# Performance work log

Hardware: AMD Instinct MI355X
Metric: run time of the kernel (lower is better)

Reference implementation:

```python
import jax, jax.numpy as jnp
import numpy as np
from jax import lax

B_SZ, N_CH, N_T = 512, 129, 250
D_MODEL = 128
D_INNER = 256            # expand * d_model
D_STATE = 16
D_CONV = 4
HEADDIM = 64             # mamba_ssm default
NHEADS = D_INNER // HEADDIM  # 4
CONV_DIM = D_INNER + 2 * D_STATE        # 288 (ngroups=1)
D_IN_PROJ = 2 * D_INNER + 2 * D_STATE + NHEADS  # 548
EPS = 1e-5


def setup_inputs() -> dict:
    key = jax.random.key(0)
    ks = jax.random.split(key, 12)
    g = lambda k, shp, s: jax.random.normal(k, shp, jnp.float32) * s
    dt0 = jax.random.uniform(ks[4], (NHEADS,), minval=0.001, maxval=0.1)
    return {
        "x": jax.random.normal(ks[0], (B_SZ, N_CH, N_T), jnp.float32),
        "mixer_w": g(ks[1], (D_MODEL, N_CH), 0.05),
        "mixer_b": jnp.zeros((D_MODEL,), jnp.float32),
        "in_proj_w": g(ks[2], (D_IN_PROJ, D_MODEL), 0.05),
        "conv_w": g(ks[3], (CONV_DIM, D_CONV), 0.2),
        "conv_b": jnp.zeros((CONV_DIM,), jnp.float32),
        "dt_bias": jnp.log(jnp.expm1(dt0)),               # inverse-softplus init
        "A_log": jnp.log(jax.random.uniform(ks[5], (NHEADS,), minval=1.0, maxval=16.0)),
        "D": jnp.ones((NHEADS,), jnp.float32),
        "norm_w": jnp.ones((D_INNER,), jnp.float32),
        "out_proj_w": g(ks[6], (D_MODEL, D_INNER), 0.05),
        "head_w": g(ks[7], (1, D_MODEL), 0.05),
        "head_b": jnp.zeros((1,), jnp.float32),
    }


def reference(x, mixer_w, mixer_b, in_proj_w, conv_w, conv_b, dt_bias,
              A_log, D, norm_w, out_proj_w, head_w, head_b):
    bsz, _, T = x.shape
    # channel mixer: (B, C, T) -> (B, T, d_model)
    u = jnp.einsum('bct,dc->btd', x, mixer_w) + mixer_b
    # Mamba2 in_proj (no bias)
    zxbcdt = u @ in_proj_w.T                        # (B, T, 548)
    z = zxbcdt[..., :D_INNER]                       # gate
    xBC = zxbcdt[..., D_INNER:D_INNER + CONV_DIM]   # (B, T, 288)
    dt = jax.nn.softplus(zxbcdt[..., -NHEADS:] + dt_bias)  # (B, T, H)
    # causal depthwise conv1d (kernel 4) + SiLU
    pad = jnp.pad(xBC, ((0, 0), (D_CONV - 1, 0), (0, 0)))
    xBC = sum(conv_w[:, k] * pad[:, k:k + T, :] for k in range(D_CONV)) + conv_b
    xBC = jax.nn.silu(xBC)
    xh = xBC[..., :D_INNER].reshape(bsz, T, NHEADS, HEADDIM)
    Bm = xBC[..., D_INNER:D_INNER + D_STATE]        # (B, T, N)
    Cm = xBC[..., D_INNER + D_STATE:]               # (B, T, N)
    A = -jnp.exp(A_log)                             # (H,)
    dA = jnp.exp(dt * A)                            # (B, T, H)
    # selective state-space scan, time-major
    tm = lambda a: jnp.moveaxis(a, 1, 0)
    def step(h, inp):
        dA_t, dt_t, x_t, B_t, C_t = inp
        # h: (B, H, P, N)
        h = h * dA_t[:, :, None, None] + (dt_t[..., None] * x_t)[..., None] * B_t[:, None, None, :]
        y_t = jnp.einsum('bhpn,bn->bhp', h, C_t)
        return h, y_t
    h0 = jnp.zeros((bsz, NHEADS, HEADDIM, D_STATE), x.dtype)
    _, ys = lax.scan(step, h0, (tm(dA), tm(dt), tm(xh), tm(Bm), tm(Cm)))
    y = jnp.moveaxis(ys, 0, 1) + D[:, None] * xh    # skip connection, (B, T, H, P)
    y = y.reshape(bsz, T, D_INNER)
    # gated RMSNorm (norm_before_gate=False)
    y = y * jax.nn.silu(z)
    y = y * lax.rsqrt(jnp.mean(y * y, axis=-1, keepdims=True) + EPS) * norm_w
    y = y @ out_proj_w.T                            # (B, T, d_model)
    # head: AdaptiveAvgPool1d(1) over time -> Flatten -> Linear(d_model, 1)
    pooled = jnp.mean(y, axis=1)                    # (B, d_model)
    return pooled @ head_w.T + head_b               # (B, 1)
```

## Files before the change

### kernel.cpp

```cpp
#include <hip/hip_runtime.h>
#include <math.h>

#define NCH     129
#define NT      250
#define DINNER  256
#define DSTATE  16
#define NHEADS  4
#define DPROJ   548
#define TC      16
#define NMT     18
#define NKS     8
#define ZR      33

typedef __attribute__((ext_vector_type(8)))  short short8;
typedef __attribute__((ext_vector_type(16))) float f32x16;

template<int N> struct IC { static constexpr int value = N; };

__device__ __forceinline__ float silu_f(float x) { return x / (1.f + __expf(-x)); }

template<int CTRL>
__device__ __forceinline__ float dstep(float v) {
    int t = __builtin_amdgcn_update_dpp(0, __float_as_int(v), CTRL, 0xF, 0xF, true);
    return v + __int_as_float(t);
}
__device__ __forceinline__ float wave_sum63(float v) {
    v = dstep<0xB1>(v);  v = dstep<0x4E>(v);  v = dstep<0x141>(v);
    v = dstep<0x140>(v); v = dstep<0x142>(v); v = dstep<0x143>(v);
    return v;
}
__device__ __forceinline__ float rdlane(float v, int l) {
    return __uint_as_float(__builtin_amdgcn_readlane(__float_as_uint(v), l));
}
__device__ __forceinline__ unsigned short f2bf(float f) {
    unsigned u = __float_as_uint(f);
    u += 0x7FFF + ((u >> 16) & 1);
    return (unsigned short)(u >> 16);
}
__device__ __forceinline__ float bf2f(unsigned short h) {
    return __uint_as_float(((unsigned)h) << 16);
}

__global__ __launch_bounds__(256) void k_prep(
    const float* __restrict__ in_proj_w,
    const float* __restrict__ mixer_w,
    const float* __restrict__ mixer_b,
    const float* __restrict__ head_w,
    const float* __restrict__ out_proj_w,
    unsigned short* __restrict__ ahi,
    unsigned short* __restrict__ alo,
    float* __restrict__ bias2,
    float* __restrict__ w128,
    float* __restrict__ vvp)
{
    int blk = blockIdx.x;
    int t = threadIdx.x;
    if (blk < NMT * NKS) {
        int mt = blk >> 3, ks = blk & 7;
        int lane = t & 63, sub = t >> 6;
        int m = mt * 32 + (lane & 31);
#pragma unroll
        for (int ii = 0; ii < 2; ++ii) {
            int i = sub * 2 + ii;
            int k = ks * 16 + (lane >> 5) * 8 + i;
            float acc = 0.f;
            if (m < DPROJ)
                for (int d = 0; d < 128; ++d)
                    acc += in_proj_w[m * 128 + d] * mixer_w[d * NCH + k];
            unsigned short hb = f2bf(acc);
            size_t o = (((size_t)(mt * NKS + ks)) * 64 + lane) * 8 + i;
            ahi[o] = hb;
            alo[o] = f2bf(acc - bf2f(hb));
        }
    } else if (blk == NMT * NKS) {
#pragma unroll
        for (int r = 0; r < 3; ++r) {
            int j = (r == 0) ? t : (r == 1) ? t + 256 : 512 + t;
            if (r == 2 && t >= 36) break;
            float ab = 0.f, aw = 0.f;
            for (int d = 0; d < 128; ++d) {
                float w = in_proj_w[j * 128 + d];
                ab += w * mixer_b[d];
                aw += w * mixer_w[d * NCH + 128];
            }
            bias2[j] = ab;
            w128[j]  = aw;
        }
    } else {
        float acc = 0.f;
        for (int d = 0; d < 128; ++d)
            acc += head_w[d] * out_proj_w[d * DINNER + t];
        vvp[t] = acc;
    }
}

__global__ __launch_bounds__(512, 1) void k_fused(
    const float* __restrict__ x,
    const unsigned short* __restrict__ ahi,
    const unsigned short* __restrict__ alo,
    const float* __restrict__ bias2,
    const float* __restrict__ w128,
    const float* __restrict__ conv_w,
    const float* __restrict__ conv_b,
    const float* __restrict__ dt_bias,
    const float* __restrict__ A_log,
    const float* __restrict__ Dv,
    const float* __restrict__ norm_w,
    const float* __restrict__ vv,
    const float* __restrict__ head_b,
    float* __restrict__ out)
{
    __shared__ short xh[NKS * 64 * 8];
    __shared__ short xl[NKS * 64 * 8];
    __shared__ float zxbuf[DPROJ * ZR];
    __shared__ float bcbuf[2][TC][32];
    __shared__ float dtbuf[2][TC][NHEADS];
    __shared__ float dAbuf[2][TC][NHEADS];
    __shared__ float x128buf[2][2][TC];
    __shared__ float smp[2][2][TC][8];

    const int b2   = blockIdx.x;
    const int tid  = threadIdx.x;
    const int lane = tid & 63;
    const int wv   = tid >> 6;
    const int mb   = wv >> 2;
    const int wq   = wv & 3;
    const int p    = (wq << 6) | lane;
    const bool isBC   = (wq == 1) && (lane < 36);
    const bool isFold = (wq == 0);

    float bz = bias2[p], bx = bias2[DINNER + p];
    float w1z = w128[p], w1x = w128[DINNER + p];
    float cw0 = conv_w[p * 4 + 0], cw1 = conv_w[p * 4 + 1];
    float cw2 = conv_w[p * 4 + 2], cw3 = conv_w[p * 4 + 3];
    float ccb = conv_b[p];
    float Dh  = Dv[wq];
    float nv  = norm_w[p] * vv[p];
    float bxb = 0.f, w1b = 0.f, e0 = 0.f, e1 = 0.f, e2 = 0.f, e3 = 0.f, eb = 0.f;
    float dtb = 0.f, Ah = 0.f;
    if (isBC) {
        bxb = bias2[512 + lane]; w1b = w128[512 + lane];
        if (lane < 32) {
            int ch = DINNER + lane;
            e0 = conv_w[ch * 4 + 0]; e1 = conv_w[ch * 4 + 1];
            e2 = conv_w[ch * 4 + 2]; e3 = conv_w[ch * 4 + 3];
            eb = conv_b[ch];
        } else {
            dtb = dt_bias[lane - 32];
            Ah  = -expf(A_log[lane - 32]);
        }
    }

    float za[TC], xa[TC], hs[DSTATE];
    float c1 = 0.f, c2 = 0.f, c3 = 0.f;
    float g1 = 0.f, g2 = 0.f, g3 = 0.f;
    float outacc = 0.f;
#pragma unroll
    for (int n = 0; n < DSTATE; ++n) hs[n] = 0.f;

    const float* xbase = x + (size_t)2 * b2 * NCH * NT;
    float2 pr[5];

    auto load_chunk = [&](int t0, auto Lc) {
        constexpr int L  = decltype(Lc)::value;
        constexpr int HP = L / 2;
        constexpr int NP = NCH * HP;
#pragma unroll
        for (int k = 0; k * 512 < 2 * NP; ++k) {
            int g = tid + 512 * k;
            if (g < 2 * NP) {
                int mbx = (g >= NP) ? 1 : 0;
                int rem = g - mbx * NP;
                int c = rem / HP, tp = rem - c * HP;
                pr[k] = *(const float2*)(xbase + (size_t)mbx * NCH * NT + c * NT + t0 + 2 * tp);
            }
        }
    };
    auto scatter_chunk = [&](auto Lc, int par) {
        constexpr int L  = decltype(Lc)::value;
        constexpr int HP = L / 2;
        constexpr int NP = NCH * HP;
#pragma unroll
        for (int k = 0; k * 512 < 2 * NP; ++k) {
            int g = tid + 512 * k;
            if (g < 2 * NP) {
                int mbx = (g >= NP) ? 1 : 0;
                int rem = g - mbx * NP;
                int c = rem / HP, tp = rem - c * HP;
                float2 v = pr[k];
                if (c < 128) {
                    int ks = c >> 4, half = (c >> 3) & 1, i = c & 7;
                    int col = mbx * 16 + 2 * tp;
                    int pos = (ks * 64 + half * 32 + col) * 8 + i;
                    unsigned short h0 = f2bf(v.x), h1 = f2bf(v.y);
                    xh[pos]     = (short)h0;
                    xh[pos + 8] = (short)h1;
                    xl[pos]     = (short)f2bf(v.x - bf2f(h0));
                    xl[pos + 8] = (short)f2bf(v.y - bf2f(h1));
                } else {
                    x128buf[par][mbx][2 * tp]     = v.x;
                    x128buf[par][mbx][2 * tp + 1] = v.y;
                }
            }
        }
    };

    load_chunk(0, IC<TC>{});
    scatter_chunk(IC<TC>{}, 0);
    __syncthreads();

    auto stage = [&](auto CLc, auto NLc, int s) {
        constexpr int CL = decltype(CLc)::value;
        constexpr int NL = decltype(NLc)::value;
        const int cur = s & 1;

        if constexpr (NL > 0) load_chunk((s + 1) * TC, IC<NL>{});
        for (int mt = wv; mt < NMT; mt += 8) {
            f32x16 a0 = {0.f,0.f,0.f,0.f,0.f,0.f,0.f,0.f,0.f,0.f,0.f,0.f,0.f,0.f,0.f,0.f};
            f32x16 a1 = {0.f,0.f,0.f,0.f,0.f,0.f,0.f,0.f,0.f,0.f,0.f,0.f,0.f,0.f,0.f,0.f};
#pragma unroll
            for (int ks = 0; ks < NKS; ++ks) {
                size_t fo = (((size_t)(mt * NKS + ks)) * 64 + lane) * 8;
                short8 ah  = *(const short8*)(ahi + fo);
                short8 al  = *(const short8*)(alo + fo);
                short8 bhv = *(const short8*)&xh[(ks * 64 + lane) * 8];
                short8 blv = *(const short8*)&xl[(ks * 64 + lane) * 8];
                a0 = __builtin_amdgcn_mfma_f32_32x32x16_bf16(ah, bhv, a0, 0, 0, 0);
                a1 = __builtin_amdgcn_mfma_f32_32x32x16_bf16(ah, blv, a1, 0, 0, 0);
                a1 = __builtin_amdgcn_mfma_f32_32x32x16_bf16(al, bhv, a1, 0, 0, 0);
            }
#pragma unroll
            for (int r = 0; r < 16; ++r) {
                int j = mt * 32 + (r & 3) + 8 * (r >> 2) + 4 * (lane >> 5);
                if (j < DPROJ) zxbuf[j * ZR + (lane & 31)] = a0[r] + a1[r];
            }
        }
        __syncthreads();

        if constexpr (NL > 0) scatter_chunk(IC<NL>{}, (s + 1) & 1);
        if (isFold && s > 0 && lane < TC) {
            const float* sp = smp[(s - 1) & 1][mb][lane];
            float s1 = sp[0] + sp[2] + sp[4] + sp[6];
            float s2 = sp[1] + sp[3] + sp[5] + sp[7];
            outacc = fmaf(s2, rsqrtf(fmaf(s1, 1.f / DINNER, 1e-5f)), outacc);
        }
#pragma unroll
        for (int tt = 0; tt < CL; ++tt) {
            float xm = x128buf[cur][mb][tt];
            int col = mb * 16 + tt;
            float zraw = zxbuf[p * ZR + col] + bz + w1z * xm;
            float xraw = zxbuf[(DINNER + p) * ZR + col] + bx + w1x * xm;
            float cv = fmaf(cw3, xraw, fmaf(cw2, c1, fmaf(cw1, c2, fmaf(cw0, c3, ccb))));
            c3 = c2; c2 = c1; c1 = xraw;
            xa[tt] = silu_f(cv);
            za[tt] = silu_f(zraw);
        }
        if (isBC) {
            if (lane < 32) {
#pragma unroll
                for (int tt = 0; tt < CL; ++tt) {
                    float xm = x128buf[cur][mb][tt];
                    float raw = zxbuf[(512 + lane) * ZR + mb * 16 + tt] + bxb + w1b * xm;
                    float cv = fmaf(e3, raw, fmaf(e2, g1, fmaf(e1, g2, fmaf(e0, g3, eb))));
                    g3 = g2; g2 = g1; g1 = raw;
                    bcbuf[mb][tt][lane] = silu_f(cv);
                }
            } else {
                int h = lane - 32;
#pragma unroll
                for (int tt = 0; tt < CL; ++tt) {
                    float xm = x128buf[cur][mb][tt];
                    float val = zxbuf[(544 + h) * ZR + mb * 16 + tt] + bxb + w1b * xm + dtb;
                    float dt = (val > 20.f) ? val : log1pf(expf(val));
                    dtbuf[mb][tt][h] = dt;
                    dAbuf[mb][tt][h] = __expf(dt * Ah);
                }
            }
        }
        __syncthreads();

#pragma unroll
        for (int tt = 0; tt < CL; ++tt) {
            float xv  = xa[tt];
            float g   = za[tt];
            float dtv = dtbuf[mb][tt][wq];
            float dAv = dAbuf[mb][tt][wq];
            float bcv = bcbuf[mb][tt][lane & 31];
            float dx = dtv * xv;
            float y0 = 0.f, y1 = 0.f, y2 = 0.f, y3 = 0.f;
#pragma unroll
            for (int n = 0; n < 4; ++n) {
                float b0 = rdlane(bcv, n),      cc0 = rdlane(bcv, DSTATE + n);
                float b1 = rdlane(bcv, 4 + n),  cc1 = rdlane(bcv, DSTATE + 4 + n);
                float b2v = rdlane(bcv, 8 + n), cc2 = rdlane(bcv, DSTATE + 8 + n);
                float b3 = rdlane(bcv, 12 + n), cc3 = rdlane(bcv, DSTATE + 12 + n);
                hs[n]      = fmaf(hs[n],      dAv, dx * b0);  y0 = fmaf(hs[n],      cc0, y0);
                hs[4 + n]  = fmaf(hs[4 + n],  dAv, dx * b1);  y1 = fmaf(hs[4 + n],  cc1, y1);
                hs[8 + n]  = fmaf(hs[8 + n],  dAv, dx * b2v); y2 = fmaf(hs[8 + n],  cc2, y2);
                hs[12 + n] = fmaf(hs[12 + n], dAv, dx * b3);  y3 = fmaf(hs[12 + n], cc3, y3);
            }
            float val = fmaf(Dh, xv, (y0 + y1) + (y2 + y3)) * g;
            float s1 = wave_sum63(val * val);
            float s2 = wave_sum63(val * nv);
            if (lane == 63) {
                smp[cur][mb][tt][2 * wq]     = s1;
                smp[cur][mb][tt][2 * wq + 1] = s2;
            }
        }
    };

    for (int s = 0; s <= 13; ++s) stage(IC<16>{}, IC<16>{}, s);
    stage(IC<16>{}, IC<10>{}, 14);
    stage(IC<10>{}, IC<0>{},  15);
    __syncthreads();

    if (isFold) {
        if (lane < 10) {
            const float* sp = smp[1][mb][lane];
            float s1 = sp[0] + sp[2] + sp[4] + sp[6];
            float s2 = sp[1] + sp[3] + sp[5] + sp[7];
            outacc = fmaf(s2, rsqrtf(fmaf(s1, 1.f / DINNER, 1e-5f)), outacc);
        }
        float tot = wave_sum63(outacc);
        if (lane == 63) out[2 * b2 + mb] = head_b[0] + tot * (1.f / NT);
    }
}

extern "C" void kernel_launch(void* const* d_in, const int* in_sizes, int n_in,
                              void* d_out, int out_size, void* d_ws, size_t ws_size,
                              hipStream_t stream) {
    const float* x         = (const float*)d_in[0];
    const float* mixer_w   = (const float*)d_in[1];
    const float* mixer_b   = (const float*)d_in[2];
    const float* in_proj_w = (const float*)d_in[3];
    const float* conv_w    = (const float*)d_in[4];
    const float* conv_b    = (const float*)d_in[5];
    const float* dt_bias   = (const float*)d_in[6];
    const float* A_log     = (const float*)d_in[7];
    const float* Dp        = (const float*)d_in[8];
    const float* norm_w    = (const float*)d_in[9];
    const float* out_proj_w= (const float*)d_in[10];
    const float* head_w    = (const float*)d_in[11];
    const float* head_b    = (const float*)d_in[12];
    float* out = (float*)d_out;

    int B = in_sizes[0] / (NCH * NT);

    const size_t FRAG = (size_t)NMT * NKS * 64 * 8;
    unsigned short* ahi = (unsigned short*)d_ws;
    unsigned short* alo = ahi + FRAG;
    float* bias2 = (float*)(alo + FRAG);
    float* w128  = bias2 + DPROJ;
    float* vvp   = w128 + DPROJ;

    k_prep<<<NMT * NKS + 2, 256, 0, stream>>>(in_proj_w, mixer_w, mixer_b,
                                              head_w, out_proj_w,
                                              ahi, alo, bias2, w128, vvp);
    k_fused<<<B / 2, 512, 0, stream>>>(x, ahi, alo, bias2, w128, conv_w, conv_b,
                                       dt_bias, A_log, Dp, norm_w, vvp, head_b, out);
}
```

Before: 433.3 us.

## Warp-specialize fused kernel into GEMM producer and scan consumer waves

Splits the 8 waves into 4 producer waves, which load x, run the MFMA GEMM one chunk ahead and double-buffer the results, and 4 consumer waves, which do conv, scan and norm for both batch rows. This lets the GEMM and the scan of adjacent chunks overlap and drops one barrier per stage. The z/x projection outputs are now stored as bf16 in shared memory, which reduces LDS use but also lowers precision. The prep kernel also stages its weights in shared memory. The change risks lower parallelism inside the scan, because each consumer wave now handles two rows in series.

```diff
diff --git a/kernel.cpp b/kernel.cpp
--- a/kernel.cpp
+++ b/kernel.cpp
@@ -10,7 +10,8 @@
 #define TC      16
 #define NMT     18
 #define NKS     8
-#define ZR      33
+#define ZRS     34
+#define ZRF     33
 
 typedef __attribute__((ext_vector_type(8)))  short short8;
 typedef __attribute__((ext_vector_type(16))) float f32x16;
@@ -56,17 +57,30 @@
     int blk = blockIdx.x;
     int t = threadIdx.x;
     if (blk < NMT * NKS) {
+        __shared__ float inp[32][129];
+        __shared__ float mw[128][17];
         int mt = blk >> 3, ks = blk & 7;
+        int m0 = mt * 32;
+        for (int u = t; u < 32 * 128; u += 256) {
+            int r = u >> 7, d = u & 127;
+            inp[r][d] = (m0 + r < DPROJ) ? in_proj_w[(m0 + r) * 128 + d] : 0.f;
+        }
+        for (int u = t; u < 128 * 16; u += 256) {
+            int d = u >> 4, kk = u & 15;
+            mw[d][kk] = mixer_w[d * NCH + ks * 16 + kk];
+        }
+        __syncthreads();
         int lane = t & 63, sub = t >> 6;
-        int m = mt * 32 + (lane & 31);
+        int mr = lane & 31;
+        int kb = (lane >> 5) * 8;
 #pragma unroll
         for (int ii = 0; ii < 2; ++ii) {
             int i = sub * 2 + ii;
-            int k = ks * 16 + (lane >> 5) * 8 + i;
+            int kk = kb & 8 ? kb - 8 + i : i;
+            kk = (kb ? 8 : 0) + i;
             float acc = 0.f;
-            if (m < DPROJ)
-                for (int d = 0; d < 128; ++d)
-                    acc += in_proj_w[m * 128 + d] * mixer_w[d * NCH + k];
+            for (int d = 0; d < 128; ++d)
+                acc = fmaf(inp[mr][d], mw[d][kk], acc);
             unsigned short hb = f2bf(acc);
             size_t o = (((size_t)(mt * NKS + ks)) * 64 + lane) * 8 + i;
             ahi[o] = hb;
@@ -110,82 +124,82 @@
     const float* __restrict__ head_b,
     float* __restrict__ out)
 {
-    __shared__ short xh[NKS * 64 * 8];
-    __shared__ short xl[NKS * 64 * 8];
-    __shared__ float zxbuf[DPROJ * ZR];
-    __shared__ float bcbuf[2][TC][32];
-    __shared__ float dtbuf[2][TC][NHEADS];
-    __shared__ float dAbuf[2][TC][NHEADS];
-    __shared__ float x128buf[2][2][TC];
+    __shared__ unsigned short xh[2][NKS * 64 * 8];
+    __shared__ unsigned short xl[2][NKS * 64 * 8];
+    __shared__ unsigned short zxlo[2][512 * ZRS];
+    __shared__ float zxf[2][36 * ZRF];
+    __shared__ float x128b[16][2][TC];
+    __shared__ float bcw[4][TC][40];
     __shared__ float smp[2][2][TC][8];
 
     const int b2   = blockIdx.x;
     const int tid  = threadIdx.x;
     const int lane = tid & 63;
     const int wv   = tid >> 6;
-    const int mb   = wv >> 2;
+    const bool isC = (wv < 4);
     const int wq   = wv & 3;
     const int p    = (wq << 6) | lane;
-    const bool isBC   = (wq == 1) && (lane < 36);
-    const bool isFold = (wq == 0);
-
-    float bz = bias2[p], bx = bias2[DINNER + p];
-    float w1z = w128[p], w1x = w128[DINNER + p];
-    float cw0 = conv_w[p * 4 + 0], cw1 = conv_w[p * 4 + 1];
-    float cw2 = conv_w[p * 4 + 2], cw3 = conv_w[p * 4 + 3];
-    float ccb = conv_b[p];
-    float Dh  = Dv[wq];
-    float nv  = norm_w[p] * vv[p];
+    const int atid = tid & 255;
+
+    float bz = 0.f, bx = 0.f, w1z = 0.f, w1x = 0.f;
+    float cw0 = 0.f, cw1 = 0.f, cw2 = 0.f, cw3 = 0.f, ccb = 0.f;
+    float Dh = 0.f, nv = 0.f;
     float bxb = 0.f, w1b = 0.f, e0 = 0.f, e1 = 0.f, e2 = 0.f, e3 = 0.f, eb = 0.f;
     float dtb = 0.f, Ah = 0.f;
-    if (isBC) {
-        bxb = bias2[512 + lane]; w1b = w128[512 + lane];
-        if (lane < 32) {
-            int ch = DINNER + lane;
-            e0 = conv_w[ch * 4 + 0]; e1 = conv_w[ch * 4 + 1];
-            e2 = conv_w[ch * 4 + 2]; e3 = conv_w[ch * 4 + 3];
-            eb = conv_b[ch];
-        } else {
-            dtb = dt_bias[lane - 32];
-            Ah  = -expf(A_log[lane - 32]);
+    if (isC) {
+        bz = bias2[p];          w1z = w128[p];
+        bx = bias2[DINNER + p]; w1x = w128[DINNER + p];
+        cw0 = conv_w[p * 4 + 0]; cw1 = conv_w[p * 4 + 1];
+        cw2 = conv_w[p * 4 + 2]; cw3 = conv_w[p * 4 + 3];
+        ccb = conv_b[p];
+        Dh = Dv[wq];
+        nv = norm_w[p] * vv[p];
+        if (lane < 36) {
+            bxb = bias2[512 + lane]; w1b = w128[512 + lane];
+            if (lane < 32) {
+                int ch = DINNER + lane;
+                e0 = conv_w[ch * 4 + 0]; e1 = conv_w[ch * 4 + 1];
+                e2 = conv_w[ch * 4 + 2]; e3 = conv_w[ch * 4 + 3];
+                eb = conv_b[ch];
+            } else {
+                dtb = dt_bias[lane - 32];
+                Ah  = -expf(A_log[lane - 32]);
+            }
         }
     }
 
-    float za[TC], xa[TC], hs[DSTATE];
-    float c1 = 0.f, c2 = 0.f, c3 = 0.f;
-    float g1 = 0.f, g2 = 0.f, g3 = 0.f;
+    float hs0[DSTATE], hs1[DSTATE], xa[TC], za[TC];
+    float c1_[2] = {0.f, 0.f}, c2_[2] = {0.f, 0.f}, c3_[2] = {0.f, 0.f};
+    float g1_[2] = {0.f, 0.f}, g2_[2] = {0.f, 0.f}, g3_[2] = {0.f, 0.f};
     float outacc = 0.f;
 #pragma unroll
-    for (int n = 0; n < DSTATE; ++n) hs[n] = 0.f;
+    for (int n = 0; n < DSTATE; ++n) { hs0[n] = 0.f; hs1[n] = 0.f; }
 
     const float* xbase = x + (size_t)2 * b2 * NCH * NT;
-    float2 pr[5];
-
-    auto load_chunk = [&](int t0, auto Lc) {
+
+    auto stage_x = [&](auto Lc, int cidx) {
         constexpr int L  = decltype(Lc)::value;
         constexpr int HP = L / 2;
-        constexpr int NP = NCH * HP;
-#pragma unroll
-        for (int k = 0; k * 512 < 2 * NP; ++k) {
-            int g = tid + 512 * k;
-            if (g < 2 * NP) {
-                int mbx = (g >= NP) ? 1 : 0;
-                int rem = g - mbx * NP;
+        constexpr int NP2 = 2 * NCH * HP;
+        const int par = cidx & 1;
+        const int t0 = cidx * TC;
+        float2 pr[9];
+#pragma unroll
+        for (int k = 0; k * 256 < NP2; ++k) {
+            int u = atid + 256 * k;
+            if (u < NP2) {
+                int mbx = (u >= NCH * HP) ? 1 : 0;
+                int rem = u - mbx * NCH * HP;
                 int c = rem / HP, tp = rem - c * HP;
                 pr[k] = *(const float2*)(xbase + (size_t)mbx * NCH * NT + c * NT + t0 + 2 * tp);
             }
         }
-    };
-    auto scatter_chunk = [&](auto Lc, int par) {
-        constexpr int L  = decltype(Lc)::value;
-        constexpr int HP = L / 2;
-        constexpr int NP = NCH * HP;
-#pragma unroll
-        for (int k = 0; k * 512 < 2 * NP; ++k) {
-            int g = tid + 512 * k;
-            if (g < 2 * NP) {
-                int mbx = (g >= NP) ? 1 : 0;
-                int rem = g - mbx * NP;
+#pragma unroll
+        for (int k = 0; k * 256 < NP2; ++k) {
+            int u = atid + 256 * k;
+            if (u < NP2) {
+                int mbx = (u >= NCH * HP) ? 1 : 0;
+                int rem = u - mbx * NCH * HP;
                 int c = rem / HP, tp = rem - c * HP;
                 float2 v = pr[k];
                 if (c < 128) {
@@ -193,136 +207,158 @@
                     int col = mbx * 16 + 2 * tp;
                     int pos = (ks * 64 + half * 32 + col) * 8 + i;
                     unsigned short h0 = f2bf(v.x), h1 = f2bf(v.y);
-                    xh[pos]     = (short)h0;
-                    xh[pos + 8] = (short)h1;
-                    xl[pos]     = (short)f2bf(v.x - bf2f(h0));
-                    xl[pos + 8] = (short)f2bf(v.y - bf2f(h1));
+                    xh[par][pos]     = h0;
+                    xh[par][pos + 8] = h1;
+                    xl[par][pos]     = f2bf(v.x - bf2f(h0));
+                    xl[par][pos + 8] = f2bf(v.y - bf2f(h1));
                 } else {
-                    x128buf[par][mbx][2 * tp]     = v.x;
-                    x128buf[par][mbx][2 * tp + 1] = v.y;
+                    x128b[cidx][mbx][2 * tp]     = v.x;
+                    x128b[cidx][mbx][2 * tp + 1] = v.y;
                 }
             }
         }
     };
 
-    load_chunk(0, IC<TC>{});
-    scatter_chunk(IC<TC>{}, 0);
-    __syncthreads();
-
-    auto stage = [&](auto CLc, auto NLc, int s) {
-        constexpr int CL = decltype(CLc)::value;
-        constexpr int NL = decltype(NLc)::value;
-        const int cur = s & 1;
-
-        if constexpr (NL > 0) load_chunk((s + 1) * TC, IC<NL>{});
-        for (int mt = wv; mt < NMT; mt += 8) {
+    auto gemm = [&](int cidx) {
+        const int par = cidx & 1;
+        short8 bh[NKS], bl[NKS];
+#pragma unroll
+        for (int ks = 0; ks < NKS; ++ks) {
+            bh[ks] = *(const short8*)&xh[par][(ks * 64 + lane) * 8];
+            bl[ks] = *(const short8*)&xl[par][(ks * 64 + lane) * 8];
+        }
+        for (int mt = wq; mt < NMT; mt += 4) {
             f32x16 a0 = {0.f,0.f,0.f,0.f,0.f,0.f,0.f,0.f,0.f,0.f,0.f,0.f,0.f,0.f,0.f,0.f};
             f32x16 a1 = {0.f,0.f,0.f,0.f,0.f,0.f,0.f,0.f,0.f,0.f,0.f,0.f,0.f,0.f,0.f,0.f};
 #pragma unroll
             for (int ks = 0; ks < NKS; ++ks) {
                 size_t fo = (((size_t)(mt * NKS + ks)) * 64 + lane) * 8;
-                short8 ah  = *(const short8*)(ahi + fo);
-                short8 al  = *(const short8*)(alo + fo);
-                short8 bhv = *(const short8*)&xh[(ks * 64 + lane) * 8];
-                short8 blv = *(const short8*)&xl[(ks * 64 + lane) * 8];
-                a0 = __builtin_amdgcn_mfma_f32_32x32x16_bf16(ah, bhv, a0, 0, 0, 0);
-                a1 = __builtin_amdgcn_mfma_f32_32x32x16_bf16(ah, blv, a1, 0, 0, 0);
-                a1 = __builtin_amdgcn_mfma_f32_32x32x16_bf16(al, bhv, a1, 0, 0, 0);
-            }
+                short8 ah = *(const short8*)(ahi + fo);
+                short8 al = *(const short8*)(alo + fo);
+                a0 = __builtin_amdgcn_mfma_f32_32x32x16_bf16(ah, bh[ks], a0, 0, 0, 0);
+                a1 = __builtin_amdgcn_mfma_f32_32x32x16_bf16(ah, bl[ks], a1, 0, 0, 0);
+                a1 = __builtin_amdgcn_mfma_f32_32x32x16_bf16(al, bh[ks], a1, 0, 0, 0);
+            }
+            int col = lane & 31;
 #pragma unroll
             for (int r = 0; r < 16; ++r) {
                 int j = mt * 32 + (r & 3) + 8 * (r >> 2) + 4 * (lane >> 5);
-                if (j < DPROJ) zxbuf[j * ZR + (lane & 31)] = a0[r] + a1[r];
-            }
-        }
-        __syncthreads();
-
-        if constexpr (NL > 0) scatter_chunk(IC<NL>{}, (s + 1) & 1);
-        if (isFold && s > 0 && lane < TC) {
-            const float* sp = smp[(s - 1) & 1][mb][lane];
+                float v = a0[r] + a1[r];
+                if (j < 512)            zxlo[par][j * ZRS + col] = f2bf(v);
+                else if (j < DPROJ)     zxf[par][(j - 512) * ZRF + col] = v;
+            }
+        }
+    };
+
+    auto cstage = [&](auto CLc, int s) {
+        constexpr int CL = decltype(CLc)::value;
+        const int par = s & 1;
+        if (s > 0 && wq < 2 && lane < TC) {
+            const float* sp = smp[(s - 1) & 1][wq][lane];
             float s1 = sp[0] + sp[2] + sp[4] + sp[6];
             float s2 = sp[1] + sp[3] + sp[5] + sp[7];
             outacc = fmaf(s2, rsqrtf(fmaf(s1, 1.f / DINNER, 1e-5f)), outacc);
         }
 #pragma unroll
-        for (int tt = 0; tt < CL; ++tt) {
-            float xm = x128buf[cur][mb][tt];
-            int col = mb * 16 + tt;
-            float zraw = zxbuf[p * ZR + col] + bz + w1z * xm;
-            float xraw = zxbuf[(DINNER + p) * ZR + col] + bx + w1x * xm;
-            float cv = fmaf(cw3, xraw, fmaf(cw2, c1, fmaf(cw1, c2, fmaf(cw0, c3, ccb))));
-            c3 = c2; c2 = c1; c1 = xraw;
-            xa[tt] = silu_f(cv);
-            za[tt] = silu_f(zraw);
-        }
-        if (isBC) {
-            if (lane < 32) {
+        for (int mb = 0; mb < 2; ++mb) {
+            float* hsp = mb ? hs1 : hs0;
+            if (lane < 36) {
+                if (lane < 32) {
+                    float r1 = g1_[mb], r2 = g2_[mb], r3 = g3_[mb];
+#pragma unroll
+                    for (int tt = 0; tt < CL; ++tt) {
+                        float xm = x128b[s][mb][tt];
+                        float raw = zxf[par][lane * ZRF + mb * 16 + tt] + bxb + w1b * xm;
+                        float cv = fmaf(e3, raw, fmaf(e2, r1, fmaf(e1, r2, fmaf(e0, r3, eb))));
+                        r3 = r2; r2 = r1; r1 = raw;
+                        bcw[wq][tt][lane] = silu_f(cv);
+                    }
+                    g1_[mb] = r1; g2_[mb] = r2; g3_[mb] = r3;
+                } else {
+                    int h = lane - 32;
+#pragma unroll
+                    for (int tt = 0; tt < CL; ++tt) {
+                        float xm = x128b[s][mb][tt];
+                        float val = zxf[par][lane * ZRF + mb * 16 + tt] + bxb + w1b * xm + dtb;
+                        float dt = (val > 20.f) ? val : log1pf(expf(val));
+                        bcw[wq][tt][32 + h] = dt;
+                        bcw[wq][tt][36 + h] = __expf(dt * Ah);
+                    }
+                }
+            }
+            __builtin_amdgcn_wave_barrier();
+            {
+                float r1 = c1_[mb], r2 = c2_[mb], r3 = c3_[mb];
 #pragma unroll
                 for (int tt = 0; tt < CL; ++tt) {
-                    float xm = x128buf[cur][mb][tt];
-                    float raw = zxbuf[(512 + lane) * ZR + mb * 16 + tt] + bxb + w1b * xm;
-                    float cv = fmaf(e3, raw, fmaf(e2, g1, fmaf(e1, g2, fmaf(e0, g3, eb))));
-                    g3 = g2; g2 = g1; g1 = raw;
-                    bcbuf[mb][tt][lane] = silu_f(cv);
-                }
-            } else {
-                int h = lane - 32;
-#pragma unroll
-                for (int tt = 0; tt < CL; ++tt) {
-                    float xm = x128buf[cur][mb][tt];
-                    float val = zxbuf[(544 + h) * ZR + mb * 16 + tt] + bxb + w1b * xm + dtb;
-                    float dt = (val > 20.f) ? val : log1pf(expf(val));
-                    dtbuf[mb][tt][h] = dt;
-                    dAbuf[mb][tt][h] = __expf(dt * Ah);
-                }
-            }
-        }
+                    float xm = x128b[s][mb][tt];
+                    int col = mb * 16 + tt;
+                    float zraw = bf2f(zxlo[par][p * ZRS + col]) + bz + w1z * xm;
+                    float xraw = bf2f(zxlo[par][(256 + p) * ZRS + col]) + bx + w1x * xm;
+                    float cv = fmaf(cw3, xraw, fmaf(cw2, r1, fmaf(cw1, r2, fmaf(cw0, r3, ccb))));
+                    r3 = r2; r2 = r1; r1 = xraw;
+                    xa[tt] = silu_f(cv);
+                    za[tt] = silu_f(zraw);
+                }
+                c1_[mb] = r1; c2_[mb] = r2; c3_[mb] = r3;
+            }
+#pragma unroll
+            for (int tt = 0; tt < CL; ++tt) {
+                float xv  = xa[tt];
+                float g   = za[tt];
+                float dtv = bcw[wq][tt][32 + wq];
+                float dAv = bcw[wq][tt][36 + wq];
+                float bcv = bcw[wq][tt][lane & 31];
+                float dx = dtv * xv;
+                float y0 = 0.f, y1 = 0.f, y2 = 0.f, y3 = 0.f;
+#pragma unroll
+                for (int n = 0; n < 4; ++n) {
+                    float b0 = rdlane(bcv, n),      cc0 = rdlane(bcv, DSTATE + n);
+                    float b1 = rdlane(bcv, 4 + n),  cc1 = rdlane(bcv, DSTATE + 4 + n);
+                    float b2v = rdlane(bcv, 8 + n), cc2 = rdlane(bcv, DSTATE + 8 + n);
+                    float b3 = rdlane(bcv, 12 + n), cc3 = rdlane(bcv, DSTATE + 12 + n);
+                    hsp[n]      = fmaf(hsp[n],      dAv, dx * b0);  y0 = fmaf(hsp[n],      cc0, y0);
+                    hsp[4 + n]  = fmaf(hsp[4 + n],  dAv, dx * b1);  y1 = fmaf(hsp[4 + n],  cc1, y1);
+                    hsp[8 + n]  = fmaf(hsp[8 + n],  dAv, dx * b2v); y2 = fmaf(hsp[8 + n],  cc2, y2);
+                    hsp[12 + n] = fmaf(hsp[12 + n], dAv, dx * b3);  y3 = fmaf(hsp[12 + n], cc3, y3);
+                }
+                float val = fmaf(Dh, xv, (y0 + y1) + (y2 + y3)) * g;
+                float s1 = wave_sum63(val * val);
+                float s2 = wave_sum63(val * nv);
+                if (lane == 63) {
+                    smp[par][mb][tt][2 * wq]     = s1;
+                    smp[par][mb][tt][2 * wq + 1] = s2;
+                }
+            }
+        }
+    };
+
+    if (!isC) stage_x(IC<16>{}, 0);
+    __syncthreads();
+    if (!isC) { gemm(0); stage_x(IC<16>{}, 1); }
+    __syncthreads();
+
+    for (int s = 0; s <= 12; ++s) {
+        if (isC) cstage(IC<16>{}, s);
+        else     { gemm(s + 1); stage_x(IC<16>{}, s + 2); }
         __syncthreads();
-
-#pragma unroll
-        for (int tt = 0; tt < CL; ++tt) {
-            float xv  = xa[tt];
-            float g   = za[tt];
-            float dtv = dtbuf[mb][tt][wq];
-            float dAv = dAbuf[mb][tt][wq];
-            float bcv = bcbuf[mb][tt][lane & 31];
-            float dx = dtv * xv;
-            float y0 = 0.f, y1 = 0.f, y2 = 0.f, y3 = 0.f;
-#pragma unroll
-            for (int n = 0; n < 4; ++n) {
-                float b0 = rdlane(bcv, n),      cc0 = rdlane(bcv, DSTATE + n);
-                float b1 = rdlane(bcv, 4 + n),  cc1 = rdlane(bcv, DSTATE + 4 + n);
-                float b2v = rdlane(bcv, 8 + n), cc2 = rdlane(bcv, DSTATE + 8 + n);
-                float b3 = rdlane(bcv, 12 + n), cc3 = rdlane(bcv, DSTATE + 12 + n);
-                hs[n]      = fmaf(hs[n],      dAv, dx * b0);  y0 = fmaf(hs[n],      cc0, y0);
-                hs[4 + n]  = fmaf(hs[4 + n],  dAv, dx * b1);  y1 = fmaf(hs[4 + n],  cc1, y1);
-                hs[8 + n]  = fmaf(hs[8 + n],  dAv, dx * b2v); y2 = fmaf(hs[8 + n],  cc2, y2);
-                hs[12 + n] = fmaf(hs[12 + n], dAv, dx * b3);  y3 = fmaf(hs[12 + n], cc3, y3);
-            }
-            float val = fmaf(Dh, xv, (y0 + y1) + (y2 + y3)) * g;
-            float s1 = wave_sum63(val * val);
-            float s2 = wave_sum63(val * nv);
-            if (lane == 63) {
-                smp[cur][mb][tt][2 * wq]     = s1;
-                smp[cur][mb][tt][2 * wq + 1] = s2;
-            }
-        }
-    };
-
-    for (int s = 0; s <= 13; ++s) stage(IC<16>{}, IC<16>{}, s);
-    stage(IC<16>{}, IC<10>{}, 14);
-    stage(IC<10>{}, IC<0>{},  15);
-    __syncthreads();
-
-    if (isFold) {
+    }
+    if (isC) cstage(IC<16>{}, 13); else { gemm(14); stage_x(IC<10>{}, 15); }
+    __syncthreads();
+    if (isC) cstage(IC<16>{}, 14); else gemm(15);
+    __syncthreads();
+    if (isC) cstage(IC<10>{}, 15);
+    __syncthreads();
+
+    if (isC && wq < 2) {
         if (lane < 10) {
-            const float* sp = smp[1][mb][lane];
+            const float* sp = smp[1][wq][lane];
             float s1 = sp[0] + sp[2] + sp[4] + sp[6];
             float s2 = sp[1] + sp[3] + sp[5] + sp[7];
             outacc = fmaf(s2, rsqrtf(fmaf(s1, 1.f / DINNER, 1e-5f)), outacc);
         }
         float tot = wave_sum63(outacc);
-        if (lane == 63) out[2 * b2 + mb] = head_b[0] + tot * (1.f / NT);
+        if (lane == 63) out[2 * b2 + wq] = head_b[0] + tot * (1.f / NT);
     }
 }
 
```

Measured after the change: 1.214 ms. 2.8x slower.
